# Optimization experiments

Hardware: AMD Instinct MI355X
Metric: run time of the kernel (lower is better)

Reference implementation:

```python
import jax, jax.numpy as jnp
import numpy as np

# Model dims
B, S, D = 4, 2048, 2048   # batch, seq, emb_dim
E, K, M = 8, 2, 1024      # num_experts, num_experts_per_tok, intermediate_dim


def setup_inputs() -> dict:
    key = jax.random.key(0)
    k0, k1, k2, k3, k4 = jax.random.split(key, 5)
    d_scale = D ** -0.5
    m_scale = M ** -0.5
    return {
        "x": jax.random.normal(k0, (B, S, D), jnp.float32),
        "w_gate": jax.random.normal(k1, (D, E), jnp.float32) * d_scale,
        "wi_0": jax.random.normal(k2, (E, D, M), jnp.float32) * d_scale,  # gate proj per expert
        "wi_1": jax.random.normal(k3, (E, D, M), jnp.float32) * d_scale,  # up proj per expert
        "wo": jax.random.normal(k4, (E, M, D), jnp.float32) * m_scale,    # down proj per expert
    }


def reference(x, w_gate, wi_0, wi_1, wo):
    b, s, d = x.shape
    e = w_gate.shape[1]
    xf = x.reshape(-1, d)                       # [T, D], T = B*S
    # --- gate logits + top-k routing ---
    logits = jnp.dot(xf, w_gate)                # [T, E]
    top_logits, top_idx = jax.lax.top_k(logits, K)    # [T, K]
    weights = jax.nn.softmax(top_logits, axis=-1)     # [T, K] router weights
    # --- sort token copies by assigned expert (dispatch) ---
    flat_idx = top_idx.reshape(-1)              # [T*K] expert id per token copy
    sort_order = jnp.argsort(flat_idx)          # [T*K] dispatch permutation
    token_ids = sort_order // K                 # source token for each sorted slot
    sorted_x = jnp.take(xf, token_ids, axis=0)  # [T*K, D] gathered activations
    group_sizes = jnp.bincount(flat_idx, length=E).astype(jnp.int32)  # tokens per expert
    # --- grouped expert GEMMs (silu-gated MLP) ---
    h0 = jax.lax.ragged_dot(sorted_x, wi_0, group_sizes)  # [T*K, M]
    h1 = jax.lax.ragged_dot(sorted_x, wi_1, group_sizes)  # [T*K, M]
    inter = jax.nn.silu(h0) * h1
    out_sorted = jax.lax.ragged_dot(inter, wo, group_sizes)  # [T*K, D]
    # --- unsort + weighted combine ---
    unsort = jnp.argsort(sort_order)
    out = jnp.take(out_sorted, unsort, axis=0).reshape(-1, K, d)  # [T, K, D]
    out = jnp.einsum("tkd,tk->td", out, weights)
    return out.reshape(b, s, d)
```

## Files before the change

### kernel.cpp

```cpp
#include <hip/hip_runtime.h>
#include <hip/hip_bf16.h>
#include <math.h>

#define T_TOK 8192
#define DIM   2048
#define NE    8
#define MDIM  1024
#define TK    16384
#define CAP   (TK + 256)
#define MAXT  72

typedef __attribute__((ext_vector_type(8))) short bf16x8;
typedef __attribute__((ext_vector_type(4))) float f32x4;

typedef __attribute__((address_space(3))) unsigned char* lds_ptr_t;
typedef const __attribute__((address_space(1))) unsigned char* glb_ptr_t;

__device__ __forceinline__ unsigned short f2bf(float f) {
  union { float f; unsigned u; } v; v.f = f;
  unsigned r = v.u + 0x7fffu + ((v.u >> 16) & 1u);
  return (unsigned short)(r >> 16);
}

__device__ __forceinline__ void gload_lds16(const void* g, void* l) {
  __builtin_amdgcn_global_load_lds((glb_ptr_t)g, (lds_ptr_t)l, 16, 0, 0);
}

#define VM_FENCE(n) asm volatile("s_waitcnt vmcnt(" #n ")" ::: "memory")
#define BARRIER() __builtin_amdgcn_s_barrier()

__device__ __forceinline__ void stage_unit(const unsigned short* __restrict__ src,
                                           int ld, unsigned char* lds, int tid) {
#pragma unroll
  for (int j = 0; j < 2; j++) {
    int idx = j * 512 + tid;
    int row = idx >> 3;
    int gslot = (idx & 7) ^ (row & 7);
    gload_lds16(src + (size_t)row * ld + gslot * 8, lds + ((idx & ~63) << 4));
  }
}

__device__ __forceinline__ bf16x8 ldsfrag(const unsigned char* base, int row, int kb) {
  return *(const bf16x8*)(base + row * 128 + (kb ^ ((row & 7) << 4)));
}

__global__ __launch_bounds__(256) void router_kernel(
    const float* __restrict__ x, const float* __restrict__ wg,
    int* __restrict__ tok_eid, float* __restrict__ tok_w) {
  __shared__ float wgT[NE][1024];
  int tid = threadIdx.x;
  int wave = tid >> 6, lane = tid & 63;
  int t0 = blockIdx.x * 16 + wave * 4;

  double acc[4][NE];
#pragma unroll
  for (int tt = 0; tt < 4; tt++)
#pragma unroll
    for (int e = 0; e < NE; e++) acc[tt][e] = 0.0;

  for (int p = 0; p < 2; p++) {
    __syncthreads();
#pragma unroll
    for (int j = tid; j < 2048; j += 256) {
      float4 v = ((const float4*)wg)[p * 2048 + j];
      int d = j >> 1, h = (j & 1) * 4;
      wgT[h + 0][d] = v.x;
      wgT[h + 1][d] = v.y;
      wgT[h + 2][d] = v.z;
      wgT[h + 3][d] = v.w;
    }
    __syncthreads();
#pragma unroll
    for (int it = 0; it < 4; it++) {
      int dd = it * 256 + lane * 4;
      int gd = p * 1024 + dd;
      float4 wf[NE];
#pragma unroll
      for (int e = 0; e < NE; e++) wf[e] = *(const float4*)&wgT[e][dd];
#pragma unroll
      for (int tt = 0; tt < 4; tt++) {
        float4 xv = *(const float4*)(x + (size_t)(t0 + tt) * DIM + gd);
#pragma unroll
        for (int e = 0; e < NE; e++) {
          acc[tt][e] += (double)xv.x * (double)wf[e].x;
          acc[tt][e] += (double)xv.y * (double)wf[e].y;
          acc[tt][e] += (double)xv.z * (double)wf[e].z;
          acc[tt][e] += (double)xv.w * (double)wf[e].w;
        }
      }
    }
  }
#pragma unroll
  for (int tt = 0; tt < 4; tt++)
#pragma unroll
    for (int e = 0; e < NE; e++) {
      double v = acc[tt][e];
#pragma unroll
      for (int off = 32; off > 0; off >>= 1) v += __shfl_down(v, off, 64);
      acc[tt][e] = v;
    }
  if (lane == 0) {
#pragma unroll
    for (int tt = 0; tt < 4; tt++) {
      int t = t0 + tt;
      int b0 = 0; double l0 = acc[tt][0];
#pragma unroll
      for (int e = 1; e < NE; e++) { if (acc[tt][e] > l0) { l0 = acc[tt][e]; b0 = e; } }
      int b1 = -1; double l1 = -1.0e300;
#pragma unroll
      for (int e = 0; e < NE; e++) { if (e != b0 && acc[tt][e] > l1) { l1 = acc[tt][e]; b1 = e; } }
      double w0 = 1.0 / (1.0 + exp(l1 - l0));
      tok_eid[2 * t]     = b0;
      tok_eid[2 * t + 1] = b1;
      tok_w[2 * t]     = (float)w0;
      tok_w[2 * t + 1] = (float)(1.0 - w0);
    }
  }
}

__global__ __launch_bounds__(256) void plan_kernel(
    const int* __restrict__ tok_eid, int* __restrict__ offsets,
    int* __restrict__ tstart, int* __restrict__ tok_slot) {
  __shared__ int cnt[256][NE];
  __shared__ int pre[256][NE];
  __shared__ int tot[NE];
  __shared__ int off_sh[NE + 1];
  int th = threadIdx.x;
  int c[NE];
#pragma unroll
  for (int k = 0; k < NE; k++) c[k] = 0;
  for (int i = 0; i < TK / 256; i++) {
    int e = tok_eid[i * 256 + th];
#pragma unroll
    for (int k = 0; k < NE; k++) c[k] += (e == k) ? 1 : 0;
  }
#pragma unroll
  for (int k = 0; k < NE; k++) cnt[th][k] = c[k];
  __syncthreads();
  if (th < NE) {
    int run = 0;
#pragma unroll 4
    for (int i = 0; i < 256; i++) { pre[i][th] = run; run += cnt[i][th]; }
    tot[th] = run;
  }
  __syncthreads();
  if (th == 0) {
    int s = 0, ts = 0;
    for (int e = 0; e < NE; e++) {
      off_sh[e] = s; offsets[e] = s; s += tot[e];
      tstart[e] = ts; ts += (tot[e] + 255) / 256;
    }
    offsets[NE] = s; off_sh[NE] = s; tstart[NE] = ts;
  }
  __syncthreads();
  int b[NE];
#pragma unroll
  for (int k = 0; k < NE; k++) b[k] = off_sh[k] + pre[th][k];
  for (int i = 0; i < TK / 256; i++) {
    int idx = i * 256 + th;
    int e = tok_eid[idx];
    int slot = 0;
#pragma unroll
    for (int k = 0; k < NE; k++) {
      slot = (e == k) ? b[k] : slot;
      b[k] += (e == k) ? 1 : 0;
    }
    tok_slot[idx] = slot;
  }
}

__global__ __launch_bounds__(256) void dispatch_kernel(
    const float* __restrict__ x, const int* __restrict__ tok_slot,
    unsigned short* __restrict__ sorted_x) {
  int t = blockIdx.x;
  size_t s0 = (size_t)tok_slot[2 * t] * DIM;
  size_t s1 = (size_t)tok_slot[2 * t + 1] * DIM;
  const float4* xr = (const float4*)(x + (size_t)t * DIM);
#pragma unroll
  for (int i = threadIdx.x; i < DIM / 4; i += 256) {
    float4 v = xr[i];
    ushort4 b;
    b.x = f2bf(v.x); b.y = f2bf(v.y); b.z = f2bf(v.z); b.w = f2bf(v.w);
    *(ushort4*)(sorted_x + s0 + (size_t)i * 4) = b;
    *(ushort4*)(sorted_x + s1 + (size_t)i * 4) = b;
  }
}

__global__ __launch_bounds__(256) void transpose_cast_kernel(
    const float* __restrict__ in, unsigned short* __restrict__ out, int R, int C) {
  __shared__ unsigned short tile[32][33];
  int e = blockIdx.z;
  const float* inp = in + (size_t)e * R * C;
  unsigned short* outp = out + (size_t)e * R * C;
  int c0 = blockIdx.x * 32, r0 = blockIdx.y * 32;
  int tx = threadIdx.x & 31, ty = threadIdx.x >> 5;
#pragma unroll
  for (int i = 0; i < 32; i += 8)
    tile[ty + i][tx] = f2bf(inp[(size_t)(r0 + ty + i) * C + (c0 + tx)]);
  __syncthreads();
#pragma unroll
  for (int i = 0; i < 32; i += 8)
    outp[(size_t)(c0 + ty + i) * R + (r0 + tx)] = tile[tx][ty + i];
}

__global__ __launch_bounds__(512, 2) void gemm12_kernel(
    const unsigned short* __restrict__ A, const unsigned short* __restrict__ W0t,
    const unsigned short* __restrict__ W1t, const int* __restrict__ offsets,
    const int* __restrict__ tstart, unsigned short* __restrict__ inter) {
  extern __shared__ unsigned char smem[];
  int bx = blockIdx.x;
  if (bx >= tstart[NE]) return;
  int e = 0;
#pragma unroll
  for (int k = 1; k < NE; k++) if (tstart[k] <= bx) e = k;
  int row0 = offsets[e], row_end = offsets[e + 1];
  int tile_r0 = row0 + (bx - tstart[e]) * 256;
  if (tile_r0 >= row_end) return;
  int colb = blockIdx.y * 128;

  int tid = threadIdx.x;
  int wave = tid >> 6, lane = tid & 63;
  int wm = wave >> 2, wn = wave & 3;
  int l15 = lane & 15, grp16 = (lane >> 4) * 16;

  const unsigned short* Ab = A + (size_t)tile_r0 * DIM;
  const unsigned short* B0b = W0t + ((size_t)e * MDIM + colb) * DIM;
  const unsigned short* B1b = W1t + ((size_t)e * MDIM + colb) * DIM;

  f32x4 acc0[8][2], acc1[8][2];
#pragma unroll
  for (int i = 0; i < 8; i++)
#pragma unroll
    for (int j = 0; j < 2; j++) {
      acc0[i][j] = (f32x4){0.f, 0.f, 0.f, 0.f};
      acc1[i][j] = (f32x4){0.f, 0.f, 0.f, 0.f};
    }
  bf16x8 af[4][2], b0f[2][2], b1f[2][2];

  stage_unit(Ab, DIM, smem + 0, tid);
  stage_unit(B0b, DIM, smem + 32768, tid);
  stage_unit(B1b, DIM, smem + 49152, tid);
  stage_unit(Ab + (size_t)128 * DIM, DIM, smem + 16384, tid);
  VM_FENCE(4);
  BARRIER();

  for (int t = 0; t < 32; t++) {
    unsigned char* S = smem + (t & 1) * 65536;
    unsigned char* P = smem + ((t & 1) ^ 1) * 65536;
    int kn = (t < 31 ? t + 1 : t) * 64;
#pragma unroll
    for (int mi = 0; mi < 4; mi++) {
      int r = wm * 64 + mi * 16 + l15;
#pragma unroll
      for (int ks = 0; ks < 2; ks++) af[mi][ks] = ldsfrag(S, r, ks * 64 + grp16);
    }
#pragma unroll
    for (int ni = 0; ni < 2; ni++) {
      int r = wn * 32 + ni * 16 + l15;
#pragma unroll
      for (int ks = 0; ks < 2; ks++) b0f[ni][ks] = ldsfrag(S + 32768, r, ks * 64 + grp16);
    }
    stage_unit(Ab + kn, DIM, P, tid);
    BARRIER();
    __builtin_amdgcn_s_setprio(1);
#pragma unroll
    for (int ks = 0; ks < 2; ks++)
#pragma unroll
      for (int mi = 0; mi < 4; mi++)
#pragma unroll
        for (int ni = 0; ni < 2; ni++)
          acc0[mi][ni] = __builtin_amdgcn_mfma_f32_16x16x32_bf16(af[mi][ks], b0f[ni][ks], acc0[mi][ni], 0, 0, 0);
    __builtin_amdgcn_s_setprio(0);
    VM_FENCE(4);
    BARRIER();
#pragma unroll
    for (int ni = 0; ni < 2; ni++) {
      int r = wn * 32 + ni * 16 + l15;
#pragma unroll
      for (int ks = 0; ks < 2; ks++) b1f[ni][ks] = ldsfrag(S + 49152, r, ks * 64 + grp16);
    }
    stage_unit(B0b + kn, DIM, P + 32768, tid);
    BARRIER();
    __builtin_amdgcn_s_setprio(1);
#pragma unroll
    for (int ks = 0; ks < 2; ks++)
#pragma unroll
      for (int mi = 0; mi < 4; mi++)
#pragma unroll
        for (int ni = 0; ni < 2; ni++)
          acc1[mi][ni] = __builtin_amdgcn_mfma_f32_16x16x32_bf16(af[mi][ks], b1f[ni][ks], acc1[mi][ni], 0, 0, 0);
    __builtin_amdgcn_s_setprio(0);
    VM_FENCE(4);
    BARRIER();
#pragma unroll
    for (int mi = 0; mi < 4; mi++) {
      int r = 128 + wm * 64 + mi * 16 + l15;
#pragma unroll
      for (int ks = 0; ks < 2; ks++) af[mi][ks] = ldsfrag(S, r, ks * 64 + grp16);
    }
    stage_unit(B1b + kn, DIM, P + 49152, tid);
    BARRIER();
    __builtin_amdgcn_s_setprio(1);
#pragma unroll
    for (int ks = 0; ks < 2; ks++)
#pragma unroll
      for (int mi = 0; mi < 4; mi++)
#pragma unroll
        for (int ni = 0; ni < 2; ni++)
          acc0[4 + mi][ni] = __builtin_amdgcn_mfma_f32_16x16x32_bf16(af[mi][ks], b0f[ni][ks], acc0[4 + mi][ni], 0, 0, 0);
    __builtin_amdgcn_s_setprio(0);
    BARRIER();
    stage_unit(Ab + (size_t)128 * DIM + kn, DIM, P + 16384, tid);
    BARRIER();
    __builtin_amdgcn_s_setprio(1);
#pragma unroll
    for (int ks = 0; ks < 2; ks++)
#pragma unroll
      for (int mi = 0; mi < 4; mi++)
#pragma unroll
        for (int ni = 0; ni < 2; ni++)
          acc1[4 + mi][ni] = __builtin_amdgcn_mfma_f32_16x16x32_bf16(af[mi][ks], b1f[ni][ks], acc1[4 + mi][ni], 0, 0, 0);
    __builtin_amdgcn_s_setprio(0);
    VM_FENCE(4);
    BARRIER();
  }
  VM_FENCE(0);

#pragma unroll
  for (int half = 0; half < 2; half++)
#pragma unroll
    for (int mi = 0; mi < 4; mi++)
#pragma unroll
      for (int reg = 0; reg < 4; reg++) {
        int grow = tile_r0 + half * 128 + wm * 64 + mi * 16 + (lane >> 4) * 4 + reg;
        if (grow < row_end) {
#pragma unroll
          for (int ni = 0; ni < 2; ni++) {
            float h0 = acc0[half * 4 + mi][ni][reg];
            float h1 = acc1[half * 4 + mi][ni][reg];
            float g = h0 / (1.0f + __expf(-h0));
            inter[(size_t)grow * MDIM + colb + wn * 32 + ni * 16 + l15] = f2bf(g * h1);
          }
        }
      }
}

__global__ __launch_bounds__(512, 2) void gemm3_kernel(
    const unsigned short* __restrict__ A, const unsigned short* __restrict__ Wot,
    const int* __restrict__ offsets, const int* __restrict__ tstart,
    float* __restrict__ out_sorted) {
  extern __shared__ unsigned char smem[];
  int bx = blockIdx.x;
  if (bx >= tstart[NE]) return;
  int e = 0;
#pragma unroll
  for (int k = 1; k < NE; k++) if (tstart[k] <= bx) e = k;
  int row0 = offsets[e], row_end = offsets[e + 1];
  int tile_r0 = row0 + (bx - tstart[e]) * 256;
  if (tile_r0 >= row_end) return;
  int col0 = blockIdx.y * 256;

  int tid = threadIdx.x;
  int wave = tid >> 6, lane = tid & 63;
  int wm = wave >> 2, wn = wave & 3;
  int l15 = lane & 15, grp16 = (lane >> 4) * 16;

  const unsigned short* Ab = A + (size_t)tile_r0 * MDIM;
  const unsigned short* Bb = Wot + ((size_t)e * DIM + col0) * MDIM;

  f32x4 acc[8][4];
#pragma unroll
  for (int i = 0; i < 8; i++)
#pragma unroll
    for (int j = 0; j < 4; j++) acc[i][j] = (f32x4){0.f, 0.f, 0.f, 0.f};
  bf16x8 af[4][2], bfr[4][2];

  stage_unit(Ab, MDIM, smem + 0, tid);
  stage_unit(Bb, MDIM, smem + 32768, tid);
  stage_unit(Bb + (size_t)128 * MDIM, MDIM, smem + 49152, tid);
  stage_unit(Ab + (size_t)128 * MDIM, MDIM, smem + 16384, tid);
  VM_FENCE(4);
  BARRIER();

  for (int t = 0; t < 16; t++) {
    unsigned char* S = smem + (t & 1) * 65536;
    unsigned char* P = smem + ((t & 1) ^ 1) * 65536;
    int kn = (t < 15 ? t + 1 : t) * 64;
#pragma unroll
    for (int mi = 0; mi < 4; mi++) {
      int r = wm * 64 + mi * 16 + l15;
#pragma unroll
      for (int ks = 0; ks < 2; ks++) af[mi][ks] = ldsfrag(S, r, ks * 64 + grp16);
    }
#pragma unroll
    for (int ni = 0; ni < 2; ni++) {
      int r = wn * 32 + ni * 16 + l15;
#pragma unroll
      for (int ks = 0; ks < 2; ks++) bfr[ni][ks] = ldsfrag(S + 32768, r, ks * 64 + grp16);
    }
    stage_unit(Ab + kn, MDIM, P, tid);
    BARRIER();
    __builtin_amdgcn_s_setprio(1);
#pragma unroll
    for (int ks = 0; ks < 2; ks++)
#pragma unroll
      for (int mi = 0; mi < 4; mi++)
#pragma unroll
        for (int ni = 0; ni < 2; ni++)
          acc[mi][ni] = __builtin_amdgcn_mfma_f32_16x16x32_bf16(af[mi][ks], bfr[ni][ks], acc[mi][ni], 0, 0, 0);
    __builtin_amdgcn_s_setprio(0);
    VM_FENCE(4);
    BARRIER();
#pragma unroll
    for (int ni = 0; ni < 2; ni++) {
      int r = 128 + wn * 32 + ni * 16 + l15;
#pragma unroll
      for (int ks = 0; ks < 2; ks++) bfr[2 + ni][ks] = ldsfrag(S + 32768, r, ks * 64 + grp16);
    }
    stage_unit(Bb + kn, MDIM, P + 32768, tid);
    BARRIER();
    __builtin_amdgcn_s_setprio(1);
#pragma unroll
    for (int ks = 0; ks < 2; ks++)
#pragma unroll
      for (int mi = 0; mi < 4; mi++)
#pragma unroll
        for (int ni = 0; ni < 2; ni++)
          acc[mi][2 + ni] = __builtin_amdgcn_mfma_f32_16x16x32_bf16(af[mi][ks], bfr[2 + ni][ks], acc[mi][2 + ni], 0, 0, 0);
    __builtin_amdgcn_s_setprio(0);
    VM_FENCE(4);
    BARRIER();
#pragma unroll
    for (int mi = 0; mi < 4; mi++) {
      int r = 128 + wm * 64 + mi * 16 + l15;
#pragma unroll
      for (int ks = 0; ks < 2; ks++) af[mi][ks] = ldsfrag(S, r, ks * 64 + grp16);
    }
    stage_unit(Bb + (size_t)128 * MDIM + kn, MDIM, P + 49152, tid);
    BARRIER();
    __builtin_amdgcn_s_setprio(1);
#pragma unroll
    for (int ks = 0; ks < 2; ks++)
#pragma unroll
      for (int mi = 0; mi < 4; mi++)
#pragma unroll
        for (int ni = 0; ni < 2; ni++)
          acc[4 + mi][ni] = __builtin_amdgcn_mfma_f32_16x16x32_bf16(af[mi][ks], bfr[ni][ks], acc[4 + mi][ni], 0, 0, 0);
    __builtin_amdgcn_s_setprio(0);
    BARRIER();
    stage_unit(Ab + (size_t)128 * MDIM + kn, MDIM, P + 16384, tid);
    BARRIER();
    __builtin_amdgcn_s_setprio(1);
#pragma unroll
    for (int ks = 0; ks < 2; ks++)
#pragma unroll
      for (int mi = 0; mi < 4; mi++)
#pragma unroll
        for (int ni = 0; ni < 2; ni++)
          acc[4 + mi][2 + ni] = __builtin_amdgcn_mfma_f32_16x16x32_bf16(af[mi][ks], bfr[2 + ni][ks], acc[4 + mi][2 + ni], 0, 0, 0);
    __builtin_amdgcn_s_setprio(0);
    VM_FENCE(4);
    BARRIER();
  }
  VM_FENCE(0);

#pragma unroll
  for (int mh = 0; mh < 2; mh++)
#pragma unroll
    for (int mi = 0; mi < 4; mi++)
#pragma unroll
      for (int reg = 0; reg < 4; reg++) {
        int grow = tile_r0 + mh * 128 + wm * 64 + mi * 16 + (lane >> 4) * 4 + reg;
        if (grow < row_end) {
#pragma unroll
          for (int nh = 0; nh < 2; nh++) {
            float* orow = out_sorted + (size_t)grow * DIM + col0 + nh * 128 + wn * 32 + l15;
#pragma unroll
            for (int ni = 0; ni < 2; ni++)
              orow[ni * 16] = acc[mh * 4 + mi][nh * 2 + ni][reg];
          }
        }
      }
}

__global__ __launch_bounds__(256) void combine_kernel(
    const float* __restrict__ os, const int* __restrict__ tok_slot,
    const float* __restrict__ tok_w, float* __restrict__ out) {
  int t = blockIdx.x * 4 + (threadIdx.x >> 6);
  int lane = threadIdx.x & 63;
  int s0 = tok_slot[2 * t], s1 = tok_slot[2 * t + 1];
  float w0 = tok_w[2 * t], w1 = tok_w[2 * t + 1];
  const float4* a = (const float4*)(os + (size_t)s0 * DIM);
  const float4* b = (const float4*)(os + (size_t)s1 * DIM);
  float4* o = (float4*)(out + (size_t)t * DIM);
#pragma unroll
  for (int i = lane; i < DIM / 4; i += 64) {
    float4 va = a[i], vb = b[i];
    float4 r;
    r.x = w0 * va.x + w1 * vb.x;
    r.y = w0 * va.y + w1 * vb.y;
    r.z = w0 * va.z + w1 * vb.z;
    r.w = w0 * va.w + w1 * vb.w;
    o[i] = r;
  }
}

extern "C" void kernel_launch(void* const* d_in, const int* in_sizes, int n_in,
                              void* d_out, int out_size, void* d_ws, size_t ws_size,
                              hipStream_t stream) {
  const float* x   = (const float*)d_in[0];
  const float* wg  = (const float*)d_in[1];
  const float* wi0 = (const float*)d_in[2];
  const float* wi1 = (const float*)d_in[3];
  const float* wo  = (const float*)d_in[4];
  float* out = (float*)d_out;

  (void)hipFuncSetAttribute(reinterpret_cast<const void*>(gemm12_kernel),
                            hipFuncAttributeMaxDynamicSharedMemorySize, 131072);
  (void)hipFuncSetAttribute(reinterpret_cast<const void*>(gemm3_kernel),
                            hipFuncAttributeMaxDynamicSharedMemorySize, 131072);

  char* ws = (char*)d_ws;
  size_t off = 0;
  auto alloc = [&](size_t bytes) -> void* {
    void* p = ws + off;
    off = (off + bytes + 255) & ~(size_t)255;
    return p;
  };
  int*   offsets  = (int*)alloc((NE + 1) * 4);
  int*   tstart   = (int*)alloc((NE + 1) * 4);
  int*   tok_eid  = (int*)alloc((size_t)2 * T_TOK * 4);
  float* tok_w    = (float*)alloc((size_t)2 * T_TOK * 4);
  int*   tok_slot = (int*)alloc((size_t)2 * T_TOK * 4);
  unsigned short* inter    = (unsigned short*)alloc((size_t)CAP * MDIM * 2);
  unsigned short* sorted_x = (unsigned short*)alloc((size_t)CAP * DIM * 2);
  unsigned short* W0t      = (unsigned short*)alloc((size_t)NE * MDIM * DIM * 2);
  unsigned short* W1t      = (unsigned short*)alloc((size_t)NE * MDIM * DIM * 2);
  unsigned short* Wot      = (unsigned short*)alloc((size_t)NE * DIM * MDIM * 2);
  float* out_sorted = (float*)sorted_x;

  router_kernel<<<T_TOK / 16, 256, 0, stream>>>(x, wg, tok_eid, tok_w);
  plan_kernel<<<1, 256, 0, stream>>>(tok_eid, offsets, tstart, tok_slot);
  dispatch_kernel<<<T_TOK, 256, 0, stream>>>(x, tok_slot, sorted_x);
  transpose_cast_kernel<<<dim3(MDIM / 32, DIM / 32, NE), 256, 0, stream>>>(wi0, W0t, DIM, MDIM);
  transpose_cast_kernel<<<dim3(MDIM / 32, DIM / 32, NE), 256, 0, stream>>>(wi1, W1t, DIM, MDIM);
  transpose_cast_kernel<<<dim3(DIM / 32, MDIM / 32, NE), 256, 0, stream>>>(wo, Wot, MDIM, DIM);

  gemm12_kernel<<<dim3(MAXT, MDIM / 128, 1), 512, 131072, stream>>>(
      sorted_x, W0t, W1t, offsets, tstart, inter);
  gemm3_kernel<<<dim3(MAXT, DIM / 256, 1), 512, 131072, stream>>>(
      inter, Wot, offsets, tstart, out_sorted);
  combine_kernel<<<T_TOK / 4, 256, 0, stream>>>(out_sorted, tok_slot, tok_w, out);
}
```

Measured before the change: 614.7 us.

## Switch expert GEMMs to 32x32x16 MFMA and issue all stage loads upfront

Both grouped GEMM kernels now use 32x32x16 bf16 MFMA tiles instead of 16x16x32, so each wave handles larger per-instruction tiles with fewer LDS fragment reads per FLOP. The main loop is restructured to issue all four global-to-LDS stage loads for the next K step at the start of each iteration, with adjusted vmcnt fences and fewer barrier phases. The epilogues are remapped to the 32x32 accumulator layout. Risks include different LDS bank-conflict behaviour for the 32-row fragment reads and correctness of the new waitcnt counts.

```diff
diff --git a/kernel.cpp b/kernel.cpp
--- a/kernel.cpp
+++ b/kernel.cpp
@@ -12,6 +12,7 @@
 
 typedef __attribute__((ext_vector_type(8))) short bf16x8;
 typedef __attribute__((ext_vector_type(4))) float f32x4;
+typedef __attribute__((ext_vector_type(16))) float f32x16;
 
 typedef __attribute__((address_space(3))) unsigned char* lds_ptr_t;
 typedef const __attribute__((address_space(1))) unsigned char* glb_ptr_t;
@@ -221,21 +222,22 @@
   int tid = threadIdx.x;
   int wave = tid >> 6, lane = tid & 63;
   int wm = wave >> 2, wn = wave & 3;
-  int l15 = lane & 15, grp16 = (lane >> 4) * 16;
+  int l31 = lane & 31;
+  int khalf = (lane >> 5) * 16;
 
   const unsigned short* Ab = A + (size_t)tile_r0 * DIM;
   const unsigned short* B0b = W0t + ((size_t)e * MDIM + colb) * DIM;
   const unsigned short* B1b = W1t + ((size_t)e * MDIM + colb) * DIM;
 
-  f32x4 acc0[8][2], acc1[8][2];
-#pragma unroll
-  for (int i = 0; i < 8; i++)
+  f32x16 acc0[2][2], acc1[2][2];
+#pragma unroll
+  for (int i = 0; i < 2; i++)
 #pragma unroll
     for (int j = 0; j < 2; j++) {
-      acc0[i][j] = (f32x4){0.f, 0.f, 0.f, 0.f};
-      acc1[i][j] = (f32x4){0.f, 0.f, 0.f, 0.f};
-    }
-  bf16x8 af[4][2], b0f[2][2], b1f[2][2];
+      acc0[i][j] = (f32x16)(0.f);
+      acc1[i][j] = (f32x16)(0.f);
+    }
+  bf16x8 af[2][4], b0f[4], b1f[4];
 
   stage_unit(Ab, DIM, smem + 0, tid);
   stage_unit(B0b, DIM, smem + 32768, tid);
@@ -248,99 +250,77 @@
     unsigned char* S = smem + (t & 1) * 65536;
     unsigned char* P = smem + ((t & 1) ^ 1) * 65536;
     int kn = (t < 31 ? t + 1 : t) * 64;
-#pragma unroll
-    for (int mi = 0; mi < 4; mi++) {
-      int r = wm * 64 + mi * 16 + l15;
-#pragma unroll
-      for (int ks = 0; ks < 2; ks++) af[mi][ks] = ldsfrag(S, r, ks * 64 + grp16);
-    }
-#pragma unroll
-    for (int ni = 0; ni < 2; ni++) {
-      int r = wn * 32 + ni * 16 + l15;
-#pragma unroll
-      for (int ks = 0; ks < 2; ks++) b0f[ni][ks] = ldsfrag(S + 32768, r, ks * 64 + grp16);
-    }
     stage_unit(Ab + kn, DIM, P, tid);
+    stage_unit(B0b + kn, DIM, P + 32768, tid);
+    stage_unit(B1b + kn, DIM, P + 49152, tid);
+    stage_unit(Ab + (size_t)128 * DIM + kn, DIM, P + 16384, tid);
+#pragma unroll
+    for (int rb = 0; rb < 2; rb++)
+#pragma unroll
+      for (int kk = 0; kk < 4; kk++)
+        af[rb][kk] = ldsfrag(S, wm * 64 + rb * 32 + l31, kk * 32 + khalf);
+#pragma unroll
+    for (int kk = 0; kk < 4; kk++)
+      b0f[kk] = ldsfrag(S + 32768, wn * 32 + l31, kk * 32 + khalf);
     BARRIER();
     __builtin_amdgcn_s_setprio(1);
 #pragma unroll
-    for (int ks = 0; ks < 2; ks++)
-#pragma unroll
-      for (int mi = 0; mi < 4; mi++)
-#pragma unroll
-        for (int ni = 0; ni < 2; ni++)
-          acc0[mi][ni] = __builtin_amdgcn_mfma_f32_16x16x32_bf16(af[mi][ks], b0f[ni][ks], acc0[mi][ni], 0, 0, 0);
+    for (int kk = 0; kk < 4; kk++)
+#pragma unroll
+      for (int rb = 0; rb < 2; rb++)
+        acc0[0][rb] = __builtin_amdgcn_mfma_f32_32x32x16_bf16(af[rb][kk], b0f[kk], acc0[0][rb], 0, 0, 0);
+    __builtin_amdgcn_s_setprio(0);
+    VM_FENCE(10);
+    BARRIER();
+#pragma unroll
+    for (int kk = 0; kk < 4; kk++)
+      b1f[kk] = ldsfrag(S + 49152, wn * 32 + l31, kk * 32 + khalf);
+    BARRIER();
+    __builtin_amdgcn_s_setprio(1);
+#pragma unroll
+    for (int kk = 0; kk < 4; kk++)
+#pragma unroll
+      for (int rb = 0; rb < 2; rb++)
+        acc1[0][rb] = __builtin_amdgcn_mfma_f32_32x32x16_bf16(af[rb][kk], b1f[kk], acc1[0][rb], 0, 0, 0);
+    __builtin_amdgcn_s_setprio(0);
+    VM_FENCE(8);
+    BARRIER();
+#pragma unroll
+    for (int rb = 0; rb < 2; rb++)
+#pragma unroll
+      for (int kk = 0; kk < 4; kk++)
+        af[rb][kk] = ldsfrag(S, 128 + wm * 64 + rb * 32 + l31, kk * 32 + khalf);
+    BARRIER();
+    __builtin_amdgcn_s_setprio(1);
+#pragma unroll
+    for (int kk = 0; kk < 4; kk++)
+#pragma unroll
+      for (int rb = 0; rb < 2; rb++)
+        acc0[1][rb] = __builtin_amdgcn_mfma_f32_32x32x16_bf16(af[rb][kk], b0f[kk], acc0[1][rb], 0, 0, 0);
+#pragma unroll
+    for (int kk = 0; kk < 4; kk++)
+#pragma unroll
+      for (int rb = 0; rb < 2; rb++)
+        acc1[1][rb] = __builtin_amdgcn_mfma_f32_32x32x16_bf16(af[rb][kk], b1f[kk], acc1[1][rb], 0, 0, 0);
     __builtin_amdgcn_s_setprio(0);
     VM_FENCE(4);
     BARRIER();
-#pragma unroll
-    for (int ni = 0; ni < 2; ni++) {
-      int r = wn * 32 + ni * 16 + l15;
-#pragma unroll
-      for (int ks = 0; ks < 2; ks++) b1f[ni][ks] = ldsfrag(S + 49152, r, ks * 64 + grp16);
-    }
-    stage_unit(B0b + kn, DIM, P + 32768, tid);
-    BARRIER();
-    __builtin_amdgcn_s_setprio(1);
-#pragma unroll
-    for (int ks = 0; ks < 2; ks++)
-#pragma unroll
-      for (int mi = 0; mi < 4; mi++)
-#pragma unroll
-        for (int ni = 0; ni < 2; ni++)
-          acc1[mi][ni] = __builtin_amdgcn_mfma_f32_16x16x32_bf16(af[mi][ks], b1f[ni][ks], acc1[mi][ni], 0, 0, 0);
-    __builtin_amdgcn_s_setprio(0);
-    VM_FENCE(4);
-    BARRIER();
-#pragma unroll
-    for (int mi = 0; mi < 4; mi++) {
-      int r = 128 + wm * 64 + mi * 16 + l15;
-#pragma unroll
-      for (int ks = 0; ks < 2; ks++) af[mi][ks] = ldsfrag(S, r, ks * 64 + grp16);
-    }
-    stage_unit(B1b + kn, DIM, P + 49152, tid);
-    BARRIER();
-    __builtin_amdgcn_s_setprio(1);
-#pragma unroll
-    for (int ks = 0; ks < 2; ks++)
-#pragma unroll
-      for (int mi = 0; mi < 4; mi++)
-#pragma unroll
-        for (int ni = 0; ni < 2; ni++)
-          acc0[4 + mi][ni] = __builtin_amdgcn_mfma_f32_16x16x32_bf16(af[mi][ks], b0f[ni][ks], acc0[4 + mi][ni], 0, 0, 0);
-    __builtin_amdgcn_s_setprio(0);
-    BARRIER();
-    stage_unit(Ab + (size_t)128 * DIM + kn, DIM, P + 16384, tid);
-    BARRIER();
-    __builtin_amdgcn_s_setprio(1);
-#pragma unroll
-    for (int ks = 0; ks < 2; ks++)
-#pragma unroll
-      for (int mi = 0; mi < 4; mi++)
-#pragma unroll
-        for (int ni = 0; ni < 2; ni++)
-          acc1[4 + mi][ni] = __builtin_amdgcn_mfma_f32_16x16x32_bf16(af[mi][ks], b1f[ni][ks], acc1[4 + mi][ni], 0, 0, 0);
-    __builtin_amdgcn_s_setprio(0);
-    VM_FENCE(4);
-    BARRIER();
   }
   VM_FENCE(0);
 
+  int rbase = 4 * (lane >> 5);
 #pragma unroll
   for (int half = 0; half < 2; half++)
 #pragma unroll
-    for (int mi = 0; mi < 4; mi++)
-#pragma unroll
-      for (int reg = 0; reg < 4; reg++) {
-        int grow = tile_r0 + half * 128 + wm * 64 + mi * 16 + (lane >> 4) * 4 + reg;
+    for (int rb = 0; rb < 2; rb++)
+#pragma unroll
+      for (int reg = 0; reg < 16; reg++) {
+        int grow = tile_r0 + half * 128 + wm * 64 + rb * 32 + (reg & 3) + 8 * (reg >> 2) + rbase;
         if (grow < row_end) {
-#pragma unroll
-          for (int ni = 0; ni < 2; ni++) {
-            float h0 = acc0[half * 4 + mi][ni][reg];
-            float h1 = acc1[half * 4 + mi][ni][reg];
-            float g = h0 / (1.0f + __expf(-h0));
-            inter[(size_t)grow * MDIM + colb + wn * 32 + ni * 16 + l15] = f2bf(g * h1);
-          }
+          float h0 = acc0[half][rb][reg];
+          float h1 = acc1[half][rb][reg];
+          float g = h0 / (1.0f + __expf(-h0));
+          inter[(size_t)grow * MDIM + colb + wn * 32 + l31] = f2bf(g * h1);
         }
       }
 }
@@ -363,17 +343,20 @@
   int tid = threadIdx.x;
   int wave = tid >> 6, lane = tid & 63;
   int wm = wave >> 2, wn = wave & 3;
-  int l15 = lane & 15, grp16 = (lane >> 4) * 16;
+  int l31 = lane & 31;
+  int khalf = (lane >> 5) * 16;
 
   const unsigned short* Ab = A + (size_t)tile_r0 * MDIM;
   const unsigned short* Bb = Wot + ((size_t)e * DIM + col0) * MDIM;
 
-  f32x4 acc[8][4];
-#pragma unroll
-  for (int i = 0; i < 8; i++)
-#pragma unroll
-    for (int j = 0; j < 4; j++) acc[i][j] = (f32x4){0.f, 0.f, 0.f, 0.f};
-  bf16x8 af[4][2], bfr[4][2];
+  f32x16 acc[2][2][2];
+#pragma unroll
+  for (int i = 0; i < 2; i++)
+#pragma unroll
+    for (int j = 0; j < 2; j++)
+#pragma unroll
+      for (int r = 0; r < 2; r++) acc[i][j][r] = (f32x16)(0.f);
+  bf16x8 af[2][4], bf0[4], bf1[4];
 
   stage_unit(Ab, MDIM, smem + 0, tid);
   stage_unit(Bb, MDIM, smem + 32768, tid);
@@ -386,99 +369,77 @@
     unsigned char* S = smem + (t & 1) * 65536;
     unsigned char* P = smem + ((t & 1) ^ 1) * 65536;
     int kn = (t < 15 ? t + 1 : t) * 64;
-#pragma unroll
-    for (int mi = 0; mi < 4; mi++) {
-      int r = wm * 64 + mi * 16 + l15;
-#pragma unroll
-      for (int ks = 0; ks < 2; ks++) af[mi][ks] = ldsfrag(S, r, ks * 64 + grp16);
-    }
-#pragma unroll
-    for (int ni = 0; ni < 2; ni++) {
-      int r = wn * 32 + ni * 16 + l15;
-#pragma unroll
-      for (int ks = 0; ks < 2; ks++) bfr[ni][ks] = ldsfrag(S + 32768, r, ks * 64 + grp16);
-    }
     stage_unit(Ab + kn, MDIM, P, tid);
+    stage_unit(Bb + kn, MDIM, P + 32768, tid);
+    stage_unit(Bb + (size_t)128 * MDIM + kn, MDIM, P + 49152, tid);
+    stage_unit(Ab + (size_t)128 * MDIM + kn, MDIM, P + 16384, tid);
+#pragma unroll
+    for (int rb = 0; rb < 2; rb++)
+#pragma unroll
+      for (int kk = 0; kk < 4; kk++)
+        af[rb][kk] = ldsfrag(S, wm * 64 + rb * 32 + l31, kk * 32 + khalf);
+#pragma unroll
+    for (int kk = 0; kk < 4; kk++)
+      bf0[kk] = ldsfrag(S + 32768, wn * 32 + l31, kk * 32 + khalf);
     BARRIER();
     __builtin_amdgcn_s_setprio(1);
 #pragma unroll
-    for (int ks = 0; ks < 2; ks++)
-#pragma unroll
-      for (int mi = 0; mi < 4; mi++)
-#pragma unroll
-        for (int ni = 0; ni < 2; ni++)
-          acc[mi][ni] = __builtin_amdgcn_mfma_f32_16x16x32_bf16(af[mi][ks], bfr[ni][ks], acc[mi][ni], 0, 0, 0);
+    for (int kk = 0; kk < 4; kk++)
+#pragma unroll
+      for (int rb = 0; rb < 2; rb++)
+        acc[0][0][rb] = __builtin_amdgcn_mfma_f32_32x32x16_bf16(af[rb][kk], bf0[kk], acc[0][0][rb], 0, 0, 0);
+    __builtin_amdgcn_s_setprio(0);
+    VM_FENCE(10);
+    BARRIER();
+#pragma unroll
+    for (int kk = 0; kk < 4; kk++)
+      bf1[kk] = ldsfrag(S + 32768, 128 + wn * 32 + l31, kk * 32 + khalf);
+    BARRIER();
+    __builtin_amdgcn_s_setprio(1);
+#pragma unroll
+    for (int kk = 0; kk < 4; kk++)
+#pragma unroll
+      for (int rb = 0; rb < 2; rb++)
+        acc[0][1][rb] = __builtin_amdgcn_mfma_f32_32x32x16_bf16(af[rb][kk], bf1[kk], acc[0][1][rb], 0, 0, 0);
+    __builtin_amdgcn_s_setprio(0);
+    VM_FENCE(8);
+    BARRIER();
+#pragma unroll
+    for (int rb = 0; rb < 2; rb++)
+#pragma unroll
+      for (int kk = 0; kk < 4; kk++)
+        af[rb][kk] = ldsfrag(S, 128 + wm * 64 + rb * 32 + l31, kk * 32 + khalf);
+    BARRIER();
+    __builtin_amdgcn_s_setprio(1);
+#pragma unroll
+    for (int kk = 0; kk < 4; kk++)
+#pragma unroll
+      for (int rb = 0; rb < 2; rb++)
+        acc[1][0][rb] = __builtin_amdgcn_mfma_f32_32x32x16_bf16(af[rb][kk], bf0[kk], acc[1][0][rb], 0, 0, 0);
+#pragma unroll
+    for (int kk = 0; kk < 4; kk++)
+#pragma unroll
+      for (int rb = 0; rb < 2; rb++)
+        acc[1][1][rb] = __builtin_amdgcn_mfma_f32_32x32x16_bf16(af[rb][kk], bf1[kk], acc[1][1][rb], 0, 0, 0);
     __builtin_amdgcn_s_setprio(0);
     VM_FENCE(4);
     BARRIER();
-#pragma unroll
-    for (int ni = 0; ni < 2; ni++) {
-      int r = 128 + wn * 32 + ni * 16 + l15;
-#pragma unroll
-      for (int ks = 0; ks < 2; ks++) bfr[2 + ni][ks] = ldsfrag(S + 32768, r, ks * 64 + grp16);
-    }
-    stage_unit(Bb + kn, MDIM, P + 32768, tid);
-    BARRIER();
-    __builtin_amdgcn_s_setprio(1);
-#pragma unroll
-    for (int ks = 0; ks < 2; ks++)
-#pragma unroll
-      for (int mi = 0; mi < 4; mi++)
-#pragma unroll
-        for (int ni = 0; ni < 2; ni++)
-          acc[mi][2 + ni] = __builtin_amdgcn_mfma_f32_16x16x32_bf16(af[mi][ks], bfr[2 + ni][ks], acc[mi][2 + ni], 0, 0, 0);
-    __builtin_amdgcn_s_setprio(0);
-    VM_FENCE(4);
-    BARRIER();
-#pragma unroll
-    for (int mi = 0; mi < 4; mi++) {
-      int r = 128 + wm * 64 + mi * 16 + l15;
-#pragma unroll
-      for (int ks = 0; ks < 2; ks++) af[mi][ks] = ldsfrag(S, r, ks * 64 + grp16);
-    }
-    stage_unit(Bb + (size_t)128 * MDIM + kn, MDIM, P + 49152, tid);
-    BARRIER();
-    __builtin_amdgcn_s_setprio(1);
-#pragma unroll
-    for (int ks = 0; ks < 2; ks++)
-#pragma unroll
-      for (int mi = 0; mi < 4; mi++)
-#pragma unroll
-        for (int ni = 0; ni < 2; ni++)
-          acc[4 + mi][ni] = __builtin_amdgcn_mfma_f32_16x16x32_bf16(af[mi][ks], bfr[ni][ks], acc[4 + mi][ni], 0, 0, 0);
-    __builtin_amdgcn_s_setprio(0);
-    BARRIER();
-    stage_unit(Ab + (size_t)128 * MDIM + kn, MDIM, P + 16384, tid);
-    BARRIER();
-    __builtin_amdgcn_s_setprio(1);
-#pragma unroll
-    for (int ks = 0; ks < 2; ks++)
-#pragma unroll
-      for (int mi = 0; mi < 4; mi++)
-#pragma unroll
-        for (int ni = 0; ni < 2; ni++)
-          acc[4 + mi][2 + ni] = __builtin_amdgcn_mfma_f32_16x16x32_bf16(af[mi][ks], bfr[2 + ni][ks], acc[4 + mi][2 + ni], 0, 0, 0);
-    __builtin_amdgcn_s_setprio(0);
-    VM_FENCE(4);
-    BARRIER();
   }
   VM_FENCE(0);
 
+  int rbase = 4 * (lane >> 5);
 #pragma unroll
   for (int mh = 0; mh < 2; mh++)
 #pragma unroll
-    for (int mi = 0; mi < 4; mi++)
-#pragma unroll
-      for (int reg = 0; reg < 4; reg++) {
-        int grow = tile_r0 + mh * 128 + wm * 64 + mi * 16 + (lane >> 4) * 4 + reg;
+    for (int rb = 0; rb < 2; rb++)
+#pragma unroll
+      for (int reg = 0; reg < 16; reg++) {
+        int grow = tile_r0 + mh * 128 + wm * 64 + rb * 32 + (reg & 3) + 8 * (reg >> 2) + rbase;
         if (grow < row_end) {
-#pragma unroll
-          for (int nh = 0; nh < 2; nh++) {
-            float* orow = out_sorted + (size_t)grow * DIM + col0 + nh * 128 + wn * 32 + l15;
-#pragma unroll
-            for (int ni = 0; ni < 2; ni++)
-              orow[ni * 16] = acc[mh * 4 + mi][nh * 2 + ni][reg];
-          }
+          float* orow = out_sorted + (size_t)grow * DIM + col0 + wn * 32 + l31;
+#pragma unroll
+          for (int nh = 0; nh < 2; nh++)
+            orow[nh * 128] = acc[mh][nh][rb][reg];
         }
       }
 }
```

Result: slower. 673.2 us (+9.5%).
